# Kernel tuning notes

Hardware: AMD Instinct MI355X
Metric: run time of the kernel (lower is better)

The kernel has to match this reference:

```python
import jax, jax.numpy as jnp
import numpy as np
import math

B, N, C, H, DC = 1, 320, 128, 4, 32  # batch, residues, pair channels, heads, per-head dim


def setup_inputs() -> dict:
    key = jax.random.key(0)
    ks = jax.random.split(key, 8)
    s = lambda k, shape: jax.random.normal(k, shape, dtype=jnp.float32) * 0.02
    return {
        "x2d": jax.random.normal(ks[0], (B, N, N, C), dtype=jnp.float32),
        "mask": jnp.ones((B, N, N), dtype=jnp.float32),
        "ln_g": jnp.ones((C,), jnp.float32),
        "ln_b": jnp.zeros((C,), jnp.float32),
        "wq": s(ks[1], (C, H * DC)),
        "wk": s(ks[2], (C, H * DC)),
        "wv": s(ks[3], (C, H * DC)),
        "wb": s(ks[4], (C, H)),
        "wg": s(ks[5], (C, H * DC)),
        "bg": jnp.zeros((H * DC,), jnp.float32),
        "wo": s(ks[6], (H * DC, C)),
        "bo": jnp.zeros((C,), jnp.float32),
    }


def reference(x2d, mask, ln_g, ln_b, wq, wk, wv, wb, wg, bg, wo, bo):
    # ending_node = False -> no transpose
    # LayerNorm (torch uses biased variance, eps=1e-5)
    mu = x2d.mean(-1, keepdims=True)
    var = ((x2d - mu) ** 2).mean(-1, keepdims=True)
    xn = (x2d - mu) * jax.lax.rsqrt(var + 1e-5) * ln_g + ln_b  # [B,N,N,C]

    sh = xn.shape[:-1]  # (B, N, N)
    q = (xn @ wq).reshape(*sh, H, DC)
    k = (xn @ wk).reshape(*sh, H, DC)
    v = (xn @ wv).reshape(*sh, H, DC)

    scale = 1.0 / math.sqrt(DC)
    aff = jnp.einsum('bmihc,bmjhc->bmhij', q * scale, k)  # [B,N,H,N,N]

    # pair bias: [B,I,J,H] -> [B,1,H,I,J], broadcast over the row axis m
    bterm = jnp.einsum('bijc,ch->bhij', xn, wb)[:, None]
    mask_bias = (100000.0 * (mask - 1.0))[:, :, None, None, :]  # [B,N,1,1,N]

    weights = jax.nn.softmax(aff + bterm + mask_bias, axis=-1)

    g = jax.nn.sigmoid((xn @ wg + bg).reshape(*sh, H, DC))
    out = jnp.einsum('bmhqk,bmkhc->bmqhc', weights, v) * g  # [B,N,N,H,DC]
    out = out.reshape(*sh, H * DC) @ wo + bo  # [B,N,N,C]
    return out
```

## Files before the change

### kernel.cpp

```cpp
#include <hip/hip_runtime.h>
#include <hip/hip_bf16.h>

typedef __attribute__((ext_vector_type(8))) short bf16x8;
typedef __attribute__((ext_vector_type(4))) float f32x4;
typedef __attribute__((ext_vector_type(4))) unsigned short u16x4;

#define DEVI static __device__ __forceinline__

DEVI float bf2f(unsigned short u) {
    union { unsigned int ui; float f; } c; c.ui = ((unsigned int)u) << 16; return c.f;
}
DEVI unsigned short f2bf(float f) {
    union { float f; unsigned int ui; } c; c.f = f;
    unsigned int u = c.ui;
    u += 0x7FFFu + ((u >> 16) & 1u);
    return (unsigned short)(u >> 16);
}
DEVI unsigned int pk2bf(float a, float b) {
    union { __hip_bfloat162 h; unsigned int u; } c;
    c.h = __float22bfloat162_rn(make_float2(a, b));
    return c.u;
}

#define NRES 320
#define NN   102400
#define CCH  128
#define NPAD 328
#define PPAD 40
#define ABLK 640

#define LOG2E 1.4426950408889634f
#define QSCALE (0.17677669529663687f * 1.4426950408889634f)

__global__ __launch_bounds__(256) void k_ln_bias(
    const float* __restrict__ x2d, const float* __restrict__ ln_g,
    const float* __restrict__ ln_b, const float* __restrict__ wb,
    unsigned short* __restrict__ xn, float* __restrict__ bterm)
{
    int wave = threadIdx.x >> 6, lane = threadIdx.x & 63;
    int r = blockIdx.x * 4 + wave;
    int c0 = lane * 2;
    float2 x = *(const float2*)(x2d + (size_t)r * CCH + c0);
    float s = x.x + x.y, sq = x.x * x.x + x.y * x.y;
    #pragma unroll
    for (int m = 1; m < 64; m <<= 1) { s += __shfl_xor(s, m, 64); sq += __shfl_xor(sq, m, 64); }
    float mu = s * (1.0f / 128.0f);
    float var = sq * (1.0f / 128.0f) - mu * mu;
    float rstd = rsqrtf(var + 1e-5f);
    float xn0 = (x.x - mu) * rstd * ln_g[c0] + ln_b[c0];
    float xn1 = (x.y - mu) * rstd * ln_g[c0 + 1] + ln_b[c0 + 1];
    *(unsigned int*)(xn + (size_t)r * CCH + c0) = pk2bf(xn0, xn1);
    float4 w0 = *(const float4*)(wb + c0 * 4);
    float4 w1 = *(const float4*)(wb + c0 * 4 + 4);
    float b0 = xn0 * w0.x + xn1 * w1.x;
    float b1 = xn0 * w0.y + xn1 * w1.y;
    float b2 = xn0 * w0.z + xn1 * w1.z;
    float b3 = xn0 * w0.w + xn1 * w1.w;
    #pragma unroll
    for (int m = 1; m < 64; m <<= 1) {
        b0 += __shfl_xor(b0, m, 64); b1 += __shfl_xor(b1, m, 64);
        b2 += __shfl_xor(b2, m, 64); b3 += __shfl_xor(b3, m, 64);
    }
    if (lane == 0) {
        bterm[0 * NN + r] = b0 * LOG2E; bterm[1 * NN + r] = b1 * LOG2E;
        bterm[2 * NN + r] = b2 * LOG2E; bterm[3 * NN + r] = b3 * LOG2E;
    }
}

__global__ __launch_bounds__(256) void k_proj(
    const unsigned short* __restrict__ xn,
    const float* __restrict__ wq, const float* __restrict__ wk,
    const float* __restrict__ wv, const float* __restrict__ wg,
    const float* __restrict__ bg,
    unsigned short* __restrict__ qkvg)
{
    __shared__ unsigned short A[128][136];
    __shared__ unsigned short Bt[128][136];
    int m0 = blockIdx.x * 128;
    int nt = blockIdx.y;
    int t = threadIdx.x;
    const float* wsrc = (nt == 0) ? wq : (nt == 1) ? wk : (nt == 2) ? wv : wg;
    #pragma unroll
    for (int it = 0; it < 8; ++it) {
        int idx = it * 256 + t;
        int row = idx >> 4, chunk = idx & 15;
        *(bf16x8*)(&A[row][chunk * 8]) = *(const bf16x8*)(xn + (size_t)(m0 + row) * CCH + chunk * 8);
    }
    {
        int n = t & 127, p = t >> 7;
        const float* col = wsrc + n;
        #pragma unroll
        for (int q = 0; q < 8; ++q) {
            int k0 = p * 64 + q * 8;
            union { unsigned int u[4]; bf16x8 v; } pk;
            #pragma unroll
            for (int z = 0; z < 4; ++z)
                pk.u[z] = pk2bf(col[(size_t)(k0 + 2 * z) * 128], col[(size_t)(k0 + 2 * z + 1) * 128]);
            *(bf16x8*)(&Bt[n][k0]) = pk.v;
        }
    }
    __syncthreads();
    int wave = t >> 6, lane = t & 63;
    int wr = (wave >> 1) * 64, wc = (wave & 1) * 64;
    int li = lane & 15, lk = (lane >> 4) * 8;
    f32x4 acc[4][4] = {};
    #pragma unroll
    for (int kk = 0; kk < 4; ++kk) {
        bf16x8 af[4], bfr[4];
        #pragma unroll
        for (int i = 0; i < 4; ++i) af[i] = *(const bf16x8*)(&A[wr + i * 16 + li][kk * 32 + lk]);
        #pragma unroll
        for (int j = 0; j < 4; ++j) bfr[j] = *(const bf16x8*)(&Bt[wc + j * 16 + li][kk * 32 + lk]);
        __builtin_amdgcn_s_setprio(1);
        #pragma unroll
        for (int i = 0; i < 4; ++i)
            #pragma unroll
            for (int j = 0; j < 4; ++j)
                acc[i][j] = __builtin_amdgcn_mfma_f32_16x16x32_bf16(af[i], bfr[j], acc[i][j], 0, 0, 0);
        __builtin_amdgcn_s_setprio(0);
    }
    int rbase = (lane >> 4) * 4;
    bool isg = (nt == 3), isq = (nt == 0);
    #pragma unroll
    for (int i = 0; i < 4; ++i) {
        #pragma unroll
        for (int j = 0; j < 4; ++j) {
            int col = wc + j * 16 + li;
            int gcol = nt * 128 + col;
            #pragma unroll
            for (int r = 0; r < 4; ++r) {
                int grow = m0 + wr + i * 16 + rbase + r;
                float v = acc[i][j][r];
                if (isg) { v += bg[col]; v = 1.0f / (1.0f + __expf(-v)); }
                if (isq) v *= QSCALE;
                qkvg[(size_t)grow * 512 + gcol] = f2bf(v);
            }
        }
    }
}

__global__ __launch_bounds__(ABLK) void k_attn(
    const unsigned short* __restrict__ qkvg,
    const float* __restrict__ bterm,
    const float* __restrict__ mask,
    unsigned short* __restrict__ opre)
{
    __shared__ unsigned short Kl[320][40];
    __shared__ unsigned short VT[32][NPAD];
    __shared__ unsigned short Pl[10][16][PPAD];
    __shared__ float mb[320];
    int bid = blockIdx.x;
    int m = bid >> 2, h = bid & 3;
    int t = threadIdx.x;
    size_t base = (size_t)m * NRES * 512;
    for (int j = t; j < NRES; j += ABLK) {
        const bf16x8* src = (const bf16x8*)(qkvg + base + (size_t)j * 512 + 128 + h * 32);
        bf16x8* dst = (bf16x8*)(&Kl[j][0]);
        dst[0] = src[0]; dst[1] = src[1]; dst[2] = src[2]; dst[3] = src[3];
    }
    {
        int dc = t & 31, jg = t >> 5;
        #pragma unroll 8
        for (int jj = 0; jj < 16; jj += 2) {
            int j = jg * 16 + jj;
            unsigned short v0 = qkvg[base + (size_t)j * 512 + 256 + h * 32 + dc];
            unsigned short v1 = qkvg[base + (size_t)(j + 1) * 512 + 256 + h * 32 + dc];
            *(unsigned int*)(&VT[dc][j]) = (unsigned int)v0 | ((unsigned int)v1 << 16);
        }
    }
    for (int j = t; j < NRES; j += ABLK) mb[j] = (100000.0f * LOG2E) * (mask[(size_t)m * NRES + j] - 1.0f);
    __syncthreads();

    int wave = t >> 6, lane = t & 63;
    int li = lane & 15, lg = lane >> 4;
    for (int c = 0; c < 2; ++c) {
        int i0 = wave * 32 + c * 16;
        int i = i0 + li;
        size_t qrow = base + (size_t)i * 512;
        bf16x8 qf = *(const bf16x8*)(qkvg + qrow + h * 32 + lg * 8);
        const float* brow = bterm + (size_t)h * NN + (size_t)i * NRES;
        f32x4 z = {0.f, 0.f, 0.f, 0.f};
        float mrun = -3.0e38f, sum = 0.0f;
        f32x4 o0 = {0.f, 0.f, 0.f, 0.f}, o1 = {0.f, 0.f, 0.f, 0.f};
        #pragma unroll 1
        for (int ph = 0; ph < 5; ++ph) {
            f32x4 st[4];
            __builtin_amdgcn_s_setprio(1);
            #pragma unroll
            for (int jf = 0; jf < 4; ++jf) {
                bf16x8 kf = *(const bf16x8*)(&Kl[ph * 64 + jf * 16 + li][lg * 8]);
                st[jf] = __builtin_amdgcn_mfma_f32_16x16x32_bf16(kf, qf, z, 0, 0, 0);
            }
            __builtin_amdgcn_s_setprio(0);
            float mx = mrun;
            #pragma unroll
            for (int jf = 0; jf < 4; ++jf) {
                int j0 = ph * 64 + jf * 16 + lg * 4;
                float4 bb = *(const float4*)(brow + j0);
                float4 mm = *(const float4*)(&mb[j0]);
                st[jf][0] += bb.x + mm.x;
                st[jf][1] += bb.y + mm.y;
                st[jf][2] += bb.z + mm.z;
                st[jf][3] += bb.w + mm.w;
                mx = fmaxf(mx, fmaxf(fmaxf(st[jf][0], st[jf][1]), fmaxf(st[jf][2], st[jf][3])));
            }
            mx = fmaxf(mx, __shfl_xor(mx, 16, 64));
            mx = fmaxf(mx, __shfl_xor(mx, 32, 64));
            if (ph) {
                float corr = __builtin_amdgcn_exp2f(mrun - mx);
                sum *= corr;
                #pragma unroll
                for (int r = 0; r < 4; ++r) { o0[r] *= corr; o1[r] *= corr; }
            }
            mrun = mx;
            #pragma unroll
            for (int half = 0; half < 2; ++half) {
                #pragma unroll
                for (int jf2 = 0; jf2 < 2; ++jf2) {
                    int jf = half * 2 + jf2;
                    float p0 = __builtin_amdgcn_exp2f(st[jf][0] - mx);
                    float p1 = __builtin_amdgcn_exp2f(st[jf][1] - mx);
                    float p2 = __builtin_amdgcn_exp2f(st[jf][2] - mx);
                    float p3 = __builtin_amdgcn_exp2f(st[jf][3] - mx);
                    sum += (p0 + p1) + (p2 + p3);
                    unsigned int* dst = (unsigned int*)(&Pl[wave][li][jf2 * 16 + lg * 4]);
                    dst[0] = pk2bf(p0, p1); dst[1] = pk2bf(p2, p3);
                }
                __builtin_amdgcn_s_setprio(1);
                {
                    bf16x8 pf = *(const bf16x8*)(&Pl[wave][li][lg * 8]);
                    bf16x8 va = *(const bf16x8*)(&VT[li][ph * 64 + half * 32 + lg * 8]);
                    bf16x8 vb = *(const bf16x8*)(&VT[16 + li][ph * 64 + half * 32 + lg * 8]);
                    o0 = __builtin_amdgcn_mfma_f32_16x16x32_bf16(va, pf, o0, 0, 0, 0);
                    o1 = __builtin_amdgcn_mfma_f32_16x16x32_bf16(vb, pf, o1, 0, 0, 0);
                }
                __builtin_amdgcn_s_setprio(0);
            }
        }
        sum += __shfl_xor(sum, 16, 64);
        sum += __shfl_xor(sum, 32, 64);
        float inv = 1.0f / sum;
        size_t orow = ((size_t)m * NRES + i) * CCH + h * 32;
        #pragma unroll
        for (int df = 0; df < 2; ++df) {
            f32x4 o = df ? o1 : o0;
            int dcb = df * 16 + lg * 4;
            u16x4 gv = *(const u16x4*)(qkvg + qrow + 384 + h * 32 + dcb);
            u16x4 ov;
            #pragma unroll
            for (int r = 0; r < 4; ++r) ov[r] = f2bf(o[r] * inv * bf2f(gv[r]));
            *(u16x4*)(opre + orow + dcb) = ov;
        }
    }
}

__global__ __launch_bounds__(256) void k_out(
    const unsigned short* __restrict__ opre, const float* __restrict__ wo,
    const float* __restrict__ bo, float* __restrict__ out)
{
    __shared__ unsigned short A[128][136];
    __shared__ unsigned short Bt[128][136];
    int m0 = blockIdx.x * 128;
    int t = threadIdx.x;
    #pragma unroll
    for (int it = 0; it < 8; ++it) {
        int idx = it * 256 + t;
        int row = idx >> 4, chunk = idx & 15;
        *(bf16x8*)(&A[row][chunk * 8]) = *(const bf16x8*)(opre + (size_t)(m0 + row) * CCH + chunk * 8);
    }
    {
        int n = t & 127, p = t >> 7;
        const float* col = wo + n;
        #pragma unroll
        for (int q = 0; q < 8; ++q) {
            int k0 = p * 64 + q * 8;
            union { unsigned int u[4]; bf16x8 v; } pk;
            #pragma unroll
            for (int z = 0; z < 4; ++z)
                pk.u[z] = pk2bf(col[(size_t)(k0 + 2 * z) * 128], col[(size_t)(k0 + 2 * z + 1) * 128]);
            *(bf16x8*)(&Bt[n][k0]) = pk.v;
        }
    }
    __syncthreads();
    int wave = t >> 6, lane = t & 63;
    int wr = (wave >> 1) * 64, wc = (wave & 1) * 64;
    int li = lane & 15, lk = (lane >> 4) * 8;
    f32x4 acc[4][4] = {};
    #pragma unroll
    for (int kk = 0; kk < 4; ++kk) {
        bf16x8 af[4], bfr[4];
        #pragma unroll
        for (int i = 0; i < 4; ++i) af[i] = *(const bf16x8*)(&A[wr + i * 16 + li][kk * 32 + lk]);
        #pragma unroll
        for (int j = 0; j < 4; ++j) bfr[j] = *(const bf16x8*)(&Bt[wc + j * 16 + li][kk * 32 + lk]);
        __builtin_amdgcn_s_setprio(1);
        #pragma unroll
        for (int i = 0; i < 4; ++i)
            #pragma unroll
            for (int j = 0; j < 4; ++j)
                acc[i][j] = __builtin_amdgcn_mfma_f32_16x16x32_bf16(af[i], bfr[j], acc[i][j], 0, 0, 0);
        __builtin_amdgcn_s_setprio(0);
    }
    int rbase = (lane >> 4) * 4;
    #pragma unroll
    for (int i = 0; i < 4; ++i) {
        #pragma unroll
        for (int j = 0; j < 4; ++j) {
            int col = wc + j * 16 + li;
            #pragma unroll
            for (int r = 0; r < 4; ++r) {
                int grow = m0 + wr + i * 16 + rbase + r;
                out[(size_t)grow * CCH + col] = acc[i][j][r] + bo[col];
            }
        }
    }
}

extern "C" void kernel_launch(void* const* d_in, const int* in_sizes, int n_in,
                              void* d_out, int out_size, void* d_ws, size_t ws_size,
                              hipStream_t stream) {
    const float* x2d  = (const float*)d_in[0];
    const float* mask = (const float*)d_in[1];
    const float* ln_g = (const float*)d_in[2];
    const float* ln_b = (const float*)d_in[3];
    const float* wq   = (const float*)d_in[4];
    const float* wk   = (const float*)d_in[5];
    const float* wv   = (const float*)d_in[6];
    const float* wb   = (const float*)d_in[7];
    const float* wg   = (const float*)d_in[8];
    const float* bg   = (const float*)d_in[9];
    const float* wo   = (const float*)d_in[10];
    const float* bo   = (const float*)d_in[11];
    float* out = (float*)d_out;

    char* ws = (char*)d_ws;
    unsigned short* xn    = (unsigned short*)ws;
    unsigned short* qkvg  = (unsigned short*)(ws + 26214400);
    float*          bterm = (float*)(ws + 26214400 + 104857600);
    unsigned short* opre  = xn;

    if (ws_size < (size_t)(26214400 + 104857600 + 1638400)) return;

    k_ln_bias<<<25600, 256, 0, stream>>>(x2d, ln_g, ln_b, wb, xn, bterm);
    k_proj<<<dim3(800, 4), 256, 0, stream>>>(xn, wq, wk, wv, wg, bg, qkvg);
    k_attn<<<1280, ABLK, 0, stream>>>(qkvg, bterm, mask, opre);
    k_out<<<800, 256, 0, stream>>>(opre, wo, bo, out);
}
```

Before: 210.5 us.

## Switch attention to 32x32 MFMA tiles with register-shuffled P, skip all-ones mask

Rewrites the attention kernel to use 32x32x16 bf16 MFMA with 32 query rows per wave and 32-key blocks. The probability tile is rearranged into the B operand with cross-lane shuffles instead of a round trip through LDS, so the P scratch buffer goes away. The block shrinks from 10 waves to 5, each doing two 32-row chunks. A block-wide flag skips the mask-bias loads when the mask is all ones, at the cost of an extra barrier and lower per-block parallelism.

```diff
diff --git a/kernel.cpp b/kernel.cpp
--- a/kernel.cpp
+++ b/kernel.cpp
@@ -3,6 +3,7 @@
 
 typedef __attribute__((ext_vector_type(8))) short bf16x8;
 typedef __attribute__((ext_vector_type(4))) float f32x4;
+typedef __attribute__((ext_vector_type(16))) float f32x16;
 typedef __attribute__((ext_vector_type(4))) unsigned short u16x4;
 
 #define DEVI static __device__ __forceinline__
@@ -26,8 +27,6 @@
 #define NN   102400
 #define CCH  128
 #define NPAD 328
-#define PPAD 40
-#define ABLK 640
 
 #define LOG2E 1.4426950408889634f
 #define QSCALE (0.17677669529663687f * 1.4426950408889634f)
@@ -139,7 +138,7 @@
     }
 }
 
-__global__ __launch_bounds__(ABLK) void k_attn(
+__global__ __launch_bounds__(320) void k_attn(
     const unsigned short* __restrict__ qkvg,
     const float* __restrict__ bterm,
     const float* __restrict__ mask,
@@ -147,108 +146,112 @@
 {
     __shared__ unsigned short Kl[320][40];
     __shared__ unsigned short VT[32][NPAD];
-    __shared__ unsigned short Pl[10][16][PPAD];
     __shared__ float mb[320];
+    __shared__ int allone;
     int bid = blockIdx.x;
     int m = bid >> 2, h = bid & 3;
     int t = threadIdx.x;
     size_t base = (size_t)m * NRES * 512;
-    for (int j = t; j < NRES; j += ABLK) {
-        const bf16x8* src = (const bf16x8*)(qkvg + base + (size_t)j * 512 + 128 + h * 32);
-        bf16x8* dst = (bf16x8*)(&Kl[j][0]);
-        dst[0] = src[0]; dst[1] = src[1]; dst[2] = src[2]; dst[3] = src[3];
+    if (t == 0) allone = 1;
+    __syncthreads();
+    for (int idx = t; idx < NRES * 4; idx += 320) {
+        int row = idx >> 2, q = idx & 3;
+        *(bf16x8*)(&Kl[row][q * 8]) =
+            *(const bf16x8*)(qkvg + base + (size_t)row * 512 + 128 + h * 32 + q * 8);
     }
     {
         int dc = t & 31, jg = t >> 5;
         #pragma unroll 8
-        for (int jj = 0; jj < 16; jj += 2) {
-            int j = jg * 16 + jj;
+        for (int jj = 0; jj < 32; jj += 2) {
+            int j = jg * 32 + jj;
             unsigned short v0 = qkvg[base + (size_t)j * 512 + 256 + h * 32 + dc];
             unsigned short v1 = qkvg[base + (size_t)(j + 1) * 512 + 256 + h * 32 + dc];
             *(unsigned int*)(&VT[dc][j]) = (unsigned int)v0 | ((unsigned int)v1 << 16);
         }
     }
-    for (int j = t; j < NRES; j += ABLK) mb[j] = (100000.0f * LOG2E) * (mask[(size_t)m * NRES + j] - 1.0f);
+    if (t < NRES) {
+        float mmv = (100000.0f * LOG2E) * (mask[(size_t)m * NRES + t] - 1.0f);
+        mb[t] = mmv;
+        if (mmv != 0.0f) allone = 0;
+    }
     __syncthreads();
+    bool nomask = (allone != 0);
 
     int wave = t >> 6, lane = t & 63;
-    int li = lane & 15, lg = lane >> 4;
+    int il = lane & 31;
+    bool hi = (lane >= 32);
+    int hi8 = hi ? 8 : 0, hi4 = hi ? 4 : 0;
     for (int c = 0; c < 2; ++c) {
-        int i0 = wave * 32 + c * 16;
-        int i = i0 + li;
+        int i = (wave * 2 + c) * 32 + il;
         size_t qrow = base + (size_t)i * 512;
-        bf16x8 qf = *(const bf16x8*)(qkvg + qrow + h * 32 + lg * 8);
+        bf16x8 qf1 = *(const bf16x8*)(qkvg + qrow + h * 32 + hi8);
+        bf16x8 qf2 = *(const bf16x8*)(qkvg + qrow + h * 32 + 16 + hi8);
         const float* brow = bterm + (size_t)h * NN + (size_t)i * NRES;
-        f32x4 z = {0.f, 0.f, 0.f, 0.f};
+        f32x16 O, z16;
+        #pragma unroll
+        for (int r = 0; r < 16; ++r) { O[r] = 0.0f; z16[r] = 0.0f; }
         float mrun = -3.0e38f, sum = 0.0f;
-        f32x4 o0 = {0.f, 0.f, 0.f, 0.f}, o1 = {0.f, 0.f, 0.f, 0.f};
         #pragma unroll 1
-        for (int ph = 0; ph < 5; ++ph) {
-            f32x4 st[4];
-            __builtin_amdgcn_s_setprio(1);
-            #pragma unroll
-            for (int jf = 0; jf < 4; ++jf) {
-                bf16x8 kf = *(const bf16x8*)(&Kl[ph * 64 + jf * 16 + li][lg * 8]);
-                st[jf] = __builtin_amdgcn_mfma_f32_16x16x32_bf16(kf, qf, z, 0, 0, 0);
+        for (int kb = 0; kb < 10; ++kb) {
+            int j0 = kb * 32;
+            bf16x8 kf1 = *(const bf16x8*)(&Kl[j0 + il][hi8]);
+            bf16x8 kf2 = *(const bf16x8*)(&Kl[j0 + il][16 + hi8]);
+            f32x16 S = __builtin_amdgcn_mfma_f32_32x32x16_bf16(kf1, qf1, z16, 0, 0, 0);
+            S = __builtin_amdgcn_mfma_f32_32x32x16_bf16(kf2, qf2, S, 0, 0, 0);
+            float mx = mrun;
+            #pragma unroll
+            for (int rg = 0; rg < 4; ++rg) {
+                float4 bb = *(const float4*)(brow + j0 + rg * 8 + hi4);
+                if (!nomask) {
+                    float4 mm = *(const float4*)(&mb[j0 + rg * 8 + hi4]);
+                    bb.x += mm.x; bb.y += mm.y; bb.z += mm.z; bb.w += mm.w;
+                }
+                S[rg * 4 + 0] += bb.x; S[rg * 4 + 1] += bb.y;
+                S[rg * 4 + 2] += bb.z; S[rg * 4 + 3] += bb.w;
+                mx = fmaxf(mx, fmaxf(fmaxf(S[rg * 4 + 0], S[rg * 4 + 1]),
+                                     fmaxf(S[rg * 4 + 2], S[rg * 4 + 3])));
             }
-            __builtin_amdgcn_s_setprio(0);
-            float mx = mrun;
-            #pragma unroll
-            for (int jf = 0; jf < 4; ++jf) {
-                int j0 = ph * 64 + jf * 16 + lg * 4;
-                float4 bb = *(const float4*)(brow + j0);
-                float4 mm = *(const float4*)(&mb[j0]);
-                st[jf][0] += bb.x + mm.x;
-                st[jf][1] += bb.y + mm.y;
-                st[jf][2] += bb.z + mm.z;
-                st[jf][3] += bb.w + mm.w;
-                mx = fmaxf(mx, fmaxf(fmaxf(st[jf][0], st[jf][1]), fmaxf(st[jf][2], st[jf][3])));
-            }
-            mx = fmaxf(mx, __shfl_xor(mx, 16, 64));
             mx = fmaxf(mx, __shfl_xor(mx, 32, 64));
-            if (ph) {
+            if (kb) {
                 float corr = __builtin_amdgcn_exp2f(mrun - mx);
                 sum *= corr;
                 #pragma unroll
-                for (int r = 0; r < 4; ++r) { o0[r] *= corr; o1[r] *= corr; }
+                for (int r = 0; r < 16; ++r) O[r] *= corr;
             }
             mrun = mx;
             #pragma unroll
-            for (int half = 0; half < 2; ++half) {
-                #pragma unroll
-                for (int jf2 = 0; jf2 < 2; ++jf2) {
-                    int jf = half * 2 + jf2;
-                    float p0 = __builtin_amdgcn_exp2f(st[jf][0] - mx);
-                    float p1 = __builtin_amdgcn_exp2f(st[jf][1] - mx);
-                    float p2 = __builtin_amdgcn_exp2f(st[jf][2] - mx);
-                    float p3 = __builtin_amdgcn_exp2f(st[jf][3] - mx);
-                    sum += (p0 + p1) + (p2 + p3);
-                    unsigned int* dst = (unsigned int*)(&Pl[wave][li][jf2 * 16 + lg * 4]);
-                    dst[0] = pk2bf(p0, p1); dst[1] = pk2bf(p2, p3);
-                }
-                __builtin_amdgcn_s_setprio(1);
-                {
-                    bf16x8 pf = *(const bf16x8*)(&Pl[wave][li][lg * 8]);
-                    bf16x8 va = *(const bf16x8*)(&VT[li][ph * 64 + half * 32 + lg * 8]);
-                    bf16x8 vb = *(const bf16x8*)(&VT[16 + li][ph * 64 + half * 32 + lg * 8]);
-                    o0 = __builtin_amdgcn_mfma_f32_16x16x32_bf16(va, pf, o0, 0, 0, 0);
-                    o1 = __builtin_amdgcn_mfma_f32_16x16x32_bf16(vb, pf, o1, 0, 0, 0);
-                }
-                __builtin_amdgcn_s_setprio(0);
-            }
-        }
-        sum += __shfl_xor(sum, 16, 64);
+            for (int r = 0; r < 16; ++r) S[r] = __builtin_amdgcn_exp2f(S[r] - mx);
+            #pragma unroll
+            for (int r = 0; r < 16; r += 4)
+                sum += (S[r] + S[r + 1]) + (S[r + 2] + S[r + 3]);
+            unsigned int w0 = pk2bf(S[0], S[1]),   w1 = pk2bf(S[2], S[3]);
+            unsigned int w2 = pk2bf(S[4], S[5]),   w3 = pk2bf(S[6], S[7]);
+            unsigned int w4 = pk2bf(S[8], S[9]),   w5 = pk2bf(S[10], S[11]);
+            unsigned int w6 = pk2bf(S[12], S[13]), w7 = pk2bf(S[14], S[15]);
+            unsigned int v02 = hi ? w0 : w2; v02 = (unsigned int)__shfl_xor((int)v02, 32, 64);
+            unsigned int v13 = hi ? w1 : w3; v13 = (unsigned int)__shfl_xor((int)v13, 32, 64);
+            unsigned int v46 = hi ? w4 : w6; v46 = (unsigned int)__shfl_xor((int)v46, 32, 64);
+            unsigned int v57 = hi ? w5 : w7; v57 = (unsigned int)__shfl_xor((int)v57, 32, 64);
+            union { unsigned int u[4]; bf16x8 v; } f1, f2;
+            f1.u[0] = hi ? v02 : w0;  f1.u[1] = hi ? v13 : w1;
+            f1.u[2] = hi ? w2 : v02;  f1.u[3] = hi ? w3 : v13;
+            f2.u[0] = hi ? v46 : w4;  f2.u[1] = hi ? v57 : w5;
+            f2.u[2] = hi ? w6 : v46;  f2.u[3] = hi ? w7 : v57;
+            bf16x8 vf1 = *(const bf16x8*)(&VT[il][j0 + hi8]);
+            bf16x8 vf2 = *(const bf16x8*)(&VT[il][j0 + 16 + hi8]);
+            O = __builtin_amdgcn_mfma_f32_32x32x16_bf16(vf1, f1.v, O, 0, 0, 0);
+            O = __builtin_amdgcn_mfma_f32_32x32x16_bf16(vf2, f2.v, O, 0, 0, 0);
+        }
         sum += __shfl_xor(sum, 32, 64);
         float inv = 1.0f / sum;
         size_t orow = ((size_t)m * NRES + i) * CCH + h * 32;
         #pragma unroll
-        for (int df = 0; df < 2; ++df) {
-            f32x4 o = df ? o1 : o0;
-            int dcb = df * 16 + lg * 4;
+        for (int rg = 0; rg < 4; ++rg) {
+            int dcb = rg * 8 + hi4;
             u16x4 gv = *(const u16x4*)(qkvg + qrow + 384 + h * 32 + dcb);
             u16x4 ov;
             #pragma unroll
-            for (int r = 0; r < 4; ++r) ov[r] = f2bf(o[r] * inv * bf2f(gv[r]));
+            for (int q = 0; q < 4; ++q) ov[q] = f2bf(O[rg * 4 + q] * inv * bf2f(gv[q]));
             *(u16x4*)(opre + orow + dcb) = ov;
         }
     }
@@ -343,6 +346,6 @@
 
     k_ln_bias<<<25600, 256, 0, stream>>>(x2d, ln_g, ln_b, wb, xn, bterm);
     k_proj<<<dim3(800, 4), 256, 0, stream>>>(xn, wq, wk, wv, wg, bg, qkvg);
-    k_attn<<<1280, ABLK, 0, stream>>>(qkvg, bterm, mask, opre);
+    k_attn<<<1280, 320, 0, stream>>>(qkvg, bterm, mask, opre);
     k_out<<<800, 256, 0, stream>>>(opre, wo, bo, out);
 }
```

After: 218.0 us. +3.6%, slower.
